# Kernel optimization log

Hardware: AMD Instinct MI355X
Metric: run time of the kernel (lower is better)

The kernel has to match this reference:

```python
import jax, jax.numpy as jnp
import numpy as np

OUT = 7   # output_size
SR = 2    # sampling_ratio
SCALES = (0.25, 0.125, 0.0625, 0.03125)  # inferred from feat sizes vs 800x800 image
K_MIN, LVL0, S0, EPS = 2, 4.0, 224.0, 1e-6


def _bilinear_gather(feat, b, y, x):
    """Legacy (aligned=False) bilinear sampling. feat [B,C,H,W]; b,y,x same shape S.
    Returns [*S, C]."""
    B, C, H, W = feat.shape
    valid = (y >= -1.0) & (y <= H) & (x >= -1.0) & (x <= W)
    y = jnp.maximum(y, 0.0)
    x = jnp.maximum(x, 0.0)
    yl = y.astype(jnp.int32)
    xl = x.astype(jnp.int32)
    ycond = yl >= H - 1
    yl = jnp.where(ycond, H - 1, yl)
    yh = jnp.where(ycond, H - 1, yl + 1)
    y = jnp.where(ycond, yl.astype(y.dtype), y)
    xcond = xl >= W - 1
    xl = jnp.where(xcond, W - 1, xl)
    xh = jnp.where(xcond, W - 1, xl + 1)
    x = jnp.where(xcond, xl.astype(x.dtype), x)
    ly = y - yl
    lx = x - xl
    hy = 1.0 - ly
    hx = 1.0 - lx
    def g(yy, xx):
        return feat[b, :, yy, xx]  # advanced indexing -> [*S, C]
    val = ((hy * hx)[..., None] * g(yl, xl)
           + (hy * lx)[..., None] * g(yl, xh)
           + (ly * hx)[..., None] * g(yh, xl)
           + (ly * lx)[..., None] * g(yh, xh))
    return jnp.where(valid[..., None], val, 0.0)


def _roi_align(feat, bidx, boxes, scale):
    """RoIAlign (aligned=False). feat [B,C,H,W], bidx [R] int, boxes [R,4] image coords.
    Returns [R,C,OUT,OUT]."""
    x1 = boxes[:, 0] * scale
    y1 = boxes[:, 1] * scale
    x2 = boxes[:, 2] * scale
    y2 = boxes[:, 3] * scale
    roi_w = jnp.maximum(x2 - x1, 1.0)
    roi_h = jnp.maximum(y2 - y1, 1.0)
    bin_h = roi_h / OUT
    bin_w = roi_w / OUT
    off = (jnp.arange(SR, dtype=feat.dtype) + 0.5) / SR      # [SR]
    ph = jnp.arange(OUT, dtype=feat.dtype)                   # [OUT]
    grid = ph[None, :, None] + off[None, None, :]            # [1,OUT,SR]
    ys = y1[:, None, None] + grid * bin_h[:, None, None]     # [R,OUT,SR]
    xs = x1[:, None, None] + grid * bin_w[:, None, None]     # [R,OUT,SR]
    Y = ys[:, :, None, :, None]                              # [R,OUT,1,SR,1]
    X = xs[:, None, :, None, :]                              # [R,1,OUT,1,SR]
    Yb, Xb = jnp.broadcast_arrays(Y, X)                      # [R,OUT,OUT,SR,SR]
    b = jnp.broadcast_to(bidx[:, None, None, None, None], Yb.shape)
    val = _bilinear_gather(feat, b, Yb, Xb)                  # [R,OUT,OUT,SR,SR,C]
    pooled = val.mean(axis=(3, 4))                           # [R,OUT,OUT,C]
    return jnp.transpose(pooled, (0, 3, 1, 2))               # [R,C,OUT,OUT]


def _levels(boxes_flat):
    """LevelMapper.run: FPN level index (0-based) per RoI."""
    area = (boxes_flat[:, 2] - boxes_flat[:, 0]) * (boxes_flat[:, 3] - boxes_flat[:, 1])
    s = jnp.sqrt(area)
    lvl = jnp.floor(LVL0 + jnp.log2(s / S0 + EPS))
    return jnp.clip(lvl, K_MIN, K_MIN + 3).astype(jnp.int32) - K_MIN


def setup_inputs() -> dict:
    key = jax.random.key(0)
    ks = jax.random.split(key, 6)
    sizes = [200, 100, 50, 25]
    inp = {f"feat{i}": jax.random.normal(ks[i], (2, 256, s, s), dtype=jnp.float32)
           for i, s in enumerate(sizes)}
    xy = jax.random.uniform(ks[4], (2, 256, 2), dtype=jnp.float32) * 500.0
    wh = jax.random.uniform(ks[5], (2, 256, 2), dtype=jnp.float32) * 400.0 + 8.0
    inp["boxes"] = jnp.concatenate([xy, xy + wh], axis=-1)  # (x1,y1,x2,y2) in [0,908)
    return inp


def reference(feat0, feat1, feat2, feat3, boxes):
    feats = [feat0, feat1, feat2, feat3]
    B, N, _ = boxes.shape
    bf = boxes.reshape(B * N, 4)
    bidx = jnp.repeat(jnp.arange(B, dtype=jnp.int32), N)  # convert_to_roi_format ids
    lv = _levels(bf)
    C = feats[0].shape[1]
    out = jnp.zeros((B * N, C, OUT, OUT), dtype=feats[0].dtype)
    for level, (f, sc) in enumerate(zip(feats, SCALES)):
        r = _roi_align(f, bidx, bf, sc)
        out = jnp.where((lv == level)[:, None, None, None], r, out)
    return out
```

## Files before the change

kernel.cpp:

```cpp
#include <hip/hip_runtime.h>

#define OUT 7
#define NCH 256
#define NROI 512
#define NS 14
#define NT 28
#define CCH 8
#define W5 5
#define WPC5 141
#define TPR (NCH * OUT * OUT)

__device__ __forceinline__ float rfl_f(float v) {
    return __int_as_float(__builtin_amdgcn_readfirstlane(__float_as_int(v)));
}

__device__ __forceinline__ unsigned int cvt_pk_bf16(float lo, float hi) {
    unsigned int r;
    asm("v_cvt_pk_bf16_f32 %0, %1, %2" : "=v"(r) : "v"(lo), "v"(hi));
    return r;
}

__global__ __launch_bounds__(256, 8) void roi_align_tap8_kernel(
        const float* __restrict__ f0, const float* __restrict__ f1,
        const float* __restrict__ f2, const float* __restrict__ f3,
        const float* __restrict__ boxes, float* __restrict__ out) {
    __shared__ __align__(16) unsigned int sm32[NT * WPC5];
    __shared__ float lyS[NS], vyS[NS], lxS[NS], vxS[NS];

    int g    = blockIdx.x;
    int xcd  = g & 7;
    int slot = g >> 3;
    int rr   = slot >> 5;
    int q    = slot & 31;
    int r    = rr * 8 + xcd;
    int tid  = (int)threadIdx.x;

    float bx1 = rfl_f(boxes[r * 4 + 0]);
    float by1 = rfl_f(boxes[r * 4 + 1]);
    float bx2 = rfl_f(boxes[r * 4 + 2]);
    float by2 = rfl_f(boxes[r * 4 + 3]);

    float area = (bx2 - bx1) * (by2 - by1);
    float s    = sqrtf(area);
    float lvl  = floorf(4.0f + log2f(s * (1.0f / 224.0f) + 1e-6f));
    lvl        = fminf(fmaxf(lvl, 2.0f), 5.0f);
    int level  = __builtin_amdgcn_readfirstlane((int)lvl - 2);

    const float* f; int H; float scale;
    switch (level) {
        case 0:  f = f0; H = 200; scale = 0.25f;    break;
        case 1:  f = f1; H = 100; scale = 0.125f;   break;
        case 2:  f = f2; H = 50;  scale = 0.0625f;  break;
        default: f = f3; H = 25;  scale = 0.03125f; break;
    }
    float Hf = (float)H;

    float x1 = bx1 * scale, y1 = by1 * scale;
    float roi_w = fmaxf(bx2 * scale - x1, 1.0f);
    float roi_h = fmaxf(by2 * scale - y1, 1.0f);
    float bin_w = roi_w * (1.0f / OUT);
    float bin_h = roi_h * (1.0f / OUT);

    int bidx = r >> 8;
    size_t HH = (size_t)(H * H);
    const float* plane = f + (size_t)(bidx * NCH + q * CCH) * HH;

    int lane = tid & 63;
    int wave = tid >> 6;
    int  j   = (lane < 28) ? lane : ((lane < 56) ? lane - 28 : lane - 56);
    int  cg  = (lane >= 28 && lane < 56) ? 1 : 0;
    bool act = (lane < 56);

    int sp = j >> 1, side = j & 1;
    int pw = sp >> 1, ixs = sp & 1;
    float xs = x1 + ((float)pw + (ixs ? 0.75f : 0.25f)) * bin_w;
    xs = fmaxf(xs, 0.0f);
    int xl = (int)xs;
    int col = (xl >= H - 1) ? (H - 1) : (xl + side);

    int roff[7];
#pragma unroll
    for (int t = 0; t < 7; ++t) {
        int rs = wave * 7 + t;
        int sy = rs >> 1;
        int ph = sy >> 1, iy = sy & 1;
        float ys = y1 + ((float)ph + (iy ? 0.75f : 0.25f)) * bin_h;
        ys = fmaxf(ys, 0.0f);
        int yl = (int)ys;
        int row = (yl >= H - 1) ? (H - 1) : (yl + (rs & 1));
        roff[t] = row * H + col;
    }

    const float* base = plane + (size_t)(cg * 4) * HH;

    float v[7][4];
#pragma unroll
    for (int t = 0; t < 7; ++t)
#pragma unroll
        for (int cc = 0; cc < 4; ++cc)
            v[t][cc] = base[(size_t)cc * HH + (size_t)roff[t]];
    asm volatile("" ::: "memory");
    __builtin_amdgcn_sched_barrier(0);

    if (tid < NS) {
        int ph = tid >> 1, iy = tid & 1;
        float y = y1 + ((float)ph + (iy ? 0.75f : 0.25f)) * bin_h;
        float vv = (y >= -1.0f && y <= Hf) ? 0.5f : 0.0f;
        y = fmaxf(y, 0.0f);
        int yl = (int)y;
        float ly = (yl >= H - 1) ? 0.0f : (y - (float)yl);
        lyS[tid] = ly; vyS[tid] = vv;
    } else if (tid >= 32 && tid < 32 + NS) {
        int t = tid - 32;
        int pw2 = t >> 1, ix2 = t & 1;
        float x = x1 + ((float)pw2 + (ix2 ? 0.75f : 0.25f)) * bin_w;
        float vv = (x >= -1.0f && x <= Hf) ? 0.5f : 0.0f;
        x = fmaxf(x, 0.0f);
        int xl2 = (int)x;
        float lx = (xl2 >= H - 1) ? 0.0f : (x - (float)xl2);
        lxS[t] = lx; vxS[t] = vv;
    }

#pragma unroll
    for (int t = 0; t < 7; ++t) {
        int rs = wave * 7 + t;
        unsigned int w01 = cvt_pk_bf16(v[t][0], v[t][1]);
        unsigned int w23 = cvt_pk_bf16(v[t][2], v[t][3]);
        if (act) {
            unsigned int* d0 = sm32 + j * WPC5 + rs * W5 + 2 * cg;
            d0[0] = w01;
            d0[1] = w23;
        }
    }
    __syncthreads();

    float accx = 0.0f, accy = 0.0f;
    int o = tid;
    if (o < 196) {
        int cp = o & 3, px = o >> 2;
        int ph = px / 7, pw2 = px - ph * 7;
        float ax = 0.0f, ay = 0.0f;
#pragma unroll
        for (int iy = 0; iy < 2; ++iy) {
            int sy = ph * 2 + iy;
            float ly = lyS[sy], hy = 1.0f - ly;
            float vy = vyS[sy];
            int r0 = (2 * sy) * W5 + cp;
            int r1 = r0 + W5;
#pragma unroll
            for (int ix = 0; ix < 2; ++ix) {
                int sx = pw2 * 2 + ix;
                float lx = lxS[sx], hx = 1.0f - lx;
                float m  = vy * vxS[sx];
                int c0i = (2 * sx) * WPC5;
                int c1i = c0i + WPC5;
                unsigned int u00 = sm32[c0i + r0];
                unsigned int u01 = sm32[c1i + r0];
                unsigned int u10 = sm32[c0i + r1];
                unsigned int u11 = sm32[c1i + r1];
                float w00 = hy * hx * m, w01 = hy * lx * m;
                float w10 = ly * hx * m, w11 = ly * lx * m;
                ax = fmaf(w00, __uint_as_float(u00 << 16), ax);
                ay = fmaf(w00, __uint_as_float(u00 & 0xFFFF0000u), ay);
                ax = fmaf(w01, __uint_as_float(u01 << 16), ax);
                ay = fmaf(w01, __uint_as_float(u01 & 0xFFFF0000u), ay);
                ax = fmaf(w10, __uint_as_float(u10 << 16), ax);
                ay = fmaf(w10, __uint_as_float(u10 & 0xFFFF0000u), ay);
                ax = fmaf(w11, __uint_as_float(u11 << 16), ax);
                ay = fmaf(w11, __uint_as_float(u11 & 0xFFFF0000u), ay);
            }
        }
        accx = ax; accy = ay;
    }
    __syncthreads();

    float* smf = (float*)sm32;
    if (o < 196) {
        int cp = o & 3, px = o >> 2;
        smf[(cp * 2 + 0) * 49 + px] = accx;
        smf[(cp * 2 + 1) * 49 + px] = accy;
    }
    __syncthreads();

    float* dst = out + (size_t)r * TPR + (size_t)q * (CCH * 49);
    if (tid < 98)
        ((float4*)dst)[tid] = ((const float4*)smf)[tid];
}

extern "C" void kernel_launch(void* const* d_in, const int* in_sizes, int n_in,
                              void* d_out, int out_size, void* d_ws, size_t ws_size,
                              hipStream_t stream) {
    const float* f0    = (const float*)d_in[0];
    const float* f1    = (const float*)d_in[1];
    const float* f2    = (const float*)d_in[2];
    const float* f3    = (const float*)d_in[3];
    const float* boxes = (const float*)d_in[4];
    float* out         = (float*)d_out;

    roi_align_tap8_kernel<<<NROI * 32, 256, 0, stream>>>(f0, f1, f2, f3, boxes, out);
}
```

Baseline: 179.0 us.

## Sort RoIs by image, level and spatial bin for cache locality; remap channel groups across XCDs

Adds a single-block bitonic sort kernel that orders RoIs by image, FPN level and a coarse 8x8 spatial cell of the box centre, writing a permutation to the workspace. The main kernel then processes RoIs in sorted order, and the block-to-work mapping now spreads one RoI's 32 channel groups across the 8 XCDs instead of pinning each RoI to one XCD. The aim is for nearby RoIs that share feature-map regions to run close together in time and hit in L2/MALL. The cost is an extra kernel launch with its serial sort, plus a dependent load of the permutation at the start of every block.

```diff
diff --git a/kernel.cpp b/kernel.cpp
--- a/kernel.cpp
+++ b/kernel.cpp
@@ -20,19 +20,64 @@
     return r;
 }
 
+__global__ __launch_bounds__(NROI) void roi_sort_kernel(
+        const float* __restrict__ boxes, int* __restrict__ perm) {
+    __shared__ unsigned int keys[NROI];
+    int i = (int)threadIdx.x;
+
+    float bx1 = boxes[i * 4 + 0], by1 = boxes[i * 4 + 1];
+    float bx2 = boxes[i * 4 + 2], by2 = boxes[i * 4 + 3];
+    float area = (bx2 - bx1) * (by2 - by1);
+    float s    = sqrtf(area);
+    float lvl  = floorf(4.0f + log2f(s * (1.0f / 224.0f) + 1e-6f));
+    lvl        = fminf(fmaxf(lvl, 2.0f), 5.0f);
+    int level  = (int)lvl - 2;
+
+    float scale, Hf;
+    switch (level) {
+        case 0:  Hf = 200.0f; scale = 0.25f;    break;
+        case 1:  Hf = 100.0f; scale = 0.125f;   break;
+        case 2:  Hf = 50.0f;  scale = 0.0625f;  break;
+        default: Hf = 25.0f;  scale = 0.03125f; break;
+    }
+    float xn = 0.5f * (bx1 + bx2) * scale / Hf;
+    float yn = 0.5f * (by1 + by2) * scale / Hf;
+    int kx = (int)(xn * 8.0f); kx = kx < 0 ? 0 : (kx > 7 ? 7 : kx);
+    int ky = (int)(yn * 8.0f); ky = ky < 0 ? 0 : (ky > 7 ? 7 : ky);
+    int img = i >> 8;
+
+    keys[i] = ((unsigned)img << 17) | ((unsigned)level << 15) |
+              ((unsigned)ky << 12)  | ((unsigned)kx << 9) | (unsigned)i;
+
+    for (unsigned k = 2; k <= NROI; k <<= 1) {
+        for (unsigned j = k >> 1; j > 0; j >>= 1) {
+            __syncthreads();
+            unsigned ixj = (unsigned)i ^ j;
+            if (ixj > (unsigned)i) {
+                unsigned a = keys[i], b = keys[ixj];
+                bool up = ((i & k) == 0);
+                if ((a > b) == up) { keys[i] = b; keys[ixj] = a; }
+            }
+        }
+    }
+    __syncthreads();
+    perm[i] = (int)(keys[i] & 511u);
+}
+
 __global__ __launch_bounds__(256, 8) void roi_align_tap8_kernel(
         const float* __restrict__ f0, const float* __restrict__ f1,
         const float* __restrict__ f2, const float* __restrict__ f3,
-        const float* __restrict__ boxes, float* __restrict__ out) {
+        const float* __restrict__ boxes, const int* __restrict__ perm,
+        float* __restrict__ out) {
     __shared__ __align__(16) unsigned int sm32[NT * WPC5];
     __shared__ float lyS[NS], vyS[NS], lxS[NS], vxS[NS];
 
     int g    = blockIdx.x;
     int xcd  = g & 7;
-    int slot = g >> 3;
-    int rr   = slot >> 5;
-    int q    = slot & 31;
-    int r    = rr * 8 + xcd;
+    int sidx = g >> 5;
+    int sub  = (g >> 3) & 3;
+    int q    = sub * 8 + xcd;
+    int r    = __builtin_amdgcn_readfirstlane(perm[sidx]);
     int tid  = (int)threadIdx.x;
 
     float bx1 = rfl_f(boxes[r * 4 + 0]);
@@ -196,6 +241,9 @@
     const float* f3    = (const float*)d_in[3];
     const float* boxes = (const float*)d_in[4];
     float* out         = (float*)d_out;
-
-    roi_align_tap8_kernel<<<NROI * 32, 256, 0, stream>>>(f0, f1, f2, f3, boxes, out);
-}
+    int*   perm        = (int*)d_ws;
+
+    roi_sort_kernel<<<1, NROI, 0, stream>>>(boxes, perm);
+    roi_align_tap8_kernel<<<NROI * 32, 256, 0, stream>>>(f0, f1, f2, f3, boxes,
+                                                         perm, out);
+}
```

Measured after the change: 179.3 us. No clear change (+0.1%).
